# Kernel optimization log

Measured on AMD Instinct MI355X. Metric: run time of the kernel, lower is better.

The kernel has to match this reference:

```python
import jax, jax.numpy as jnp
import numpy as np

NUM_HEADS = 12
HEAD_DIM = 64
HIDDEN = 768
QMAX = 127.0  # 8-bit symmetric
DOMAIN_MIN, DOMAIN_MAX = -10.0, 0.0
NUM_INTERVALS = 12


def _build_pla_coeffs():
    xs = np.linspace(DOMAIN_MIN, DOMAIN_MAX, 1001)
    ys = np.exp(xs)
    intervals = np.linspace(DOMAIN_MIN, DOMAIN_MAX, NUM_INTERVALS + 1)
    ms, cs = [], []
    for i in range(NUM_INTERVALS):
        a, b = intervals[i], intervals[i + 1]
        mask = (xs >= a) & (xs <= b)
        m, c = np.polyfit(xs[mask], ys[mask], 1)
        ms.append(m)
        cs.append(c)
    return (jnp.asarray(ms, jnp.float32), jnp.asarray(cs, jnp.float32),
            jnp.asarray(intervals, jnp.float32))

COEFFS_M, COEFFS_C, INTERVALS = _build_pla_coeffs()


def quantize(x):
    # per-row (last-dim) abs-max symmetric 8-bit fake quant
    max_val = jnp.max(jnp.abs(x), axis=-1, keepdims=True)
    scale = max_val / QMAX
    scale = jnp.where(scale == 0, 1.0, scale)
    return jnp.clip(jnp.round(x / scale), -QMAX, QMAX) * scale


def to_fixed_point(x, bits=32, frac_bits=26):
    scale = 2.0 ** frac_bits
    lo = -2.0 ** (bits - 1)
    hi = 2.0 ** (bits - 1) - 1
    return jnp.clip(jnp.round(x * scale), lo, hi) / scale


def pla_exp(x):
    xc = jnp.clip(x, DOMAIN_MIN, DOMAIN_MAX)
    # sum(x >= intervals) - 1 == searchsorted(intervals, x, 'right') - 1
    idx = jnp.clip(jnp.searchsorted(INTERVALS, xc, side='right') - 1, 0, NUM_INTERVALS - 1)
    return COEFFS_M[idx] * xc + COEFFS_C[idx]


def pla_softmax(scores):
    shifted = scores - jnp.max(scores, axis=-1, keepdims=True)
    shifted_fx = to_fixed_point(shifted, 32, 26)
    exps = pla_exp(shifted_fx)
    sm = exps / (jnp.sum(exps, axis=-1, keepdims=True) + 1e-9)
    return quantize(sm)


def q_linear(x, W, b):
    # QuantizedLinear: quantize input and weight (per-row), fp bias
    return quantize(x) @ quantize(W).T + b


def split_heads(x):
    B, S, _ = x.shape
    return x.reshape(B, S, NUM_HEADS, HEAD_DIM).transpose(0, 2, 1, 3)  # bhsd


def mhsa(hidden_states, Wq, bq, Wk, bk, Wv, bv, Wo, bo):
    B, S, H = hidden_states.shape
    scale = HEAD_DIM ** -0.5
    q = split_heads(q_linear(hidden_states, Wq, bq))
    k = split_heads(q_linear(hidden_states, Wk, bk))
    v = split_heads(q_linear(hidden_states, Wv, bv))
    # per-row quantization makes tile-wise quant identical to full quant
    scores = jnp.einsum('bhqd,bhkd->bhqk', quantize(q), quantize(k)) * scale
    probs = pla_softmax(scores)
    ctx = jnp.einsum('bhqk,bhkd->bhqd', probs, quantize(v))
    ctx = ctx.transpose(0, 2, 1, 3).reshape(B, S, H)
    return q_linear(ctx, Wo, bo)


def setup_inputs() -> dict:
    key = jax.random.key(0)
    ks = jax.random.split(key, 9)
    B, S = 8, 512
    hs = jax.random.normal(ks[0], (B, S, HIDDEN), dtype=jnp.float32)
    def w(k):
        return jax.random.normal(k, (HIDDEN, HIDDEN), dtype=jnp.float32) * 0.02
    def b(k):
        return jax.random.normal(k, (HIDDEN,), dtype=jnp.float32) * 0.02
    return {
        'hidden_states': hs,
        'Wq': w(ks[1]), 'bq': b(ks[2]),
        'Wk': w(ks[3]), 'bk': b(ks[4]),
        'Wv': w(ks[5]), 'bv': b(ks[6]),
        'Wo': w(ks[7]), 'bo': b(ks[8]),
    }


def reference(hidden_states, Wq, bq, Wk, bk, Wv, bv, Wo, bo):
    return mhsa(hidden_states, Wq, bq, Wk, bk, Wv, bv, Wo, bo)
```

## Files before the change

### kernel.cpp

```cpp
#include <hip/hip_runtime.h>
#include <cmath>

#define R_TOT 4096
#define HID   768
#define NHEAD 12
#define HDIM  64
#define SEQ   512
#define BATCH 8

typedef int   v4i  __attribute__((ext_vector_type(4)));
typedef float v4f  __attribute__((ext_vector_type(4)));
typedef _Float16 half8 __attribute__((ext_vector_type(8)));
typedef _Float16 half4v __attribute__((ext_vector_type(4)));

__device__ __forceinline__ void gl_lds16(const signed char* g, signed char* l) {
  __builtin_amdgcn_global_load_lds(
      (const __attribute__((address_space(1))) void*)g,
      (__attribute__((address_space(3))) void*)l, 16, 0, 0);
}

struct PlaConsts { float m[12]; float c[12]; float b[13]; };

static PlaConsts build_pla() {
  PlaConsts pc;
  const int NPTS = 1001;
  static double xs[NPTS], ys[NPTS];
  const double step = 10.0 / 1000.0;
  for (int j = 0; j < NPTS; ++j) xs[j] = (double)j * step + (-10.0);
  xs[NPTS - 1] = 0.0;
  for (int j = 0; j < NPTS; ++j) ys[j] = std::exp(xs[j]);
  double bnd[13];
  const double step2 = 10.0 / 12.0;
  for (int k = 0; k < 13; ++k) bnd[k] = (double)k * step2 + (-10.0);
  bnd[12] = 0.0;
  for (int i = 0; i < 12; ++i) {
    const double a = bnd[i], bb = bnd[i + 1];
    double sx = 0, sy = 0; int n = 0;
    for (int j = 0; j < NPTS; ++j)
      if (xs[j] >= a && xs[j] <= bb) { sx += xs[j]; sy += ys[j]; ++n; }
    const double xm = sx / n, ym = sy / n;
    double sxx = 0, sxy = 0;
    for (int j = 0; j < NPTS; ++j)
      if (xs[j] >= a && xs[j] <= bb) {
        const double dx = xs[j] - xm;
        sxx += dx * dx; sxy += dx * (ys[j] - ym);
      }
    const double m = sxy / sxx;
    pc.m[i] = (float)m;
    pc.c[i] = (float)(ym - m * xm);
  }
  for (int k = 0; k < 13; ++k) pc.b[k] = (float)bnd[k];
  return pc;
}
static const PlaConsts g_pla = build_pla();

__device__ __forceinline__ void quant_row_wave(const float* __restrict__ x,
                                               signed char* __restrict__ qrow,
                                               float* __restrict__ srow) {
  const int lane = threadIdx.x & 63;
  const float4* x4 = (const float4*)x;
  const float4 a = x4[lane];
  const float4 b = x4[lane + 64];
  const float4 c = x4[lane + 128];
  float m = fmaxf(fmaxf(fabsf(a.x), fabsf(a.y)), fmaxf(fabsf(a.z), fabsf(a.w)));
  m = fmaxf(m, fmaxf(fmaxf(fabsf(b.x), fabsf(b.y)), fmaxf(fabsf(b.z), fabsf(b.w))));
  m = fmaxf(m, fmaxf(fmaxf(fabsf(c.x), fabsf(c.y)), fmaxf(fabsf(c.z), fabsf(c.w))));
  #pragma unroll
  for (int off = 32; off; off >>= 1) m = fmaxf(m, __shfl_xor(m, off));
  float s = m / 127.0f;
  if (s == 0.f) s = 1.f;
  auto qb = [&](float v) -> int {
    return ((int)fminf(fmaxf(rintf(v / s), -127.f), 127.f)) & 255;
  };
  const int p0 = qb(a.x) | (qb(a.y) << 8) | (qb(a.z) << 16) | (qb(a.w) << 24);
  const int p1 = qb(b.x) | (qb(b.y) << 8) | (qb(b.z) << 16) | (qb(b.w) << 24);
  const int p2 = qb(c.x) | (qb(c.y) << 8) | (qb(c.z) << 16) | (qb(c.w) << 24);
  int* q4 = (int*)qrow;
  q4[lane] = p0;
  q4[lane + 64] = p1;
  q4[lane + 128] = p2;
  if (lane == 0) *srow = s;
}

__global__ __launch_bounds__(256)
void quant_rows(const float* __restrict__ src,
                signed char* __restrict__ qout, float* __restrict__ sout) {
  const int row = blockIdx.x * 4 + (threadIdx.x >> 6);
  quant_row_wave(src + (size_t)row * HID, qout + (size_t)row * HID, sout + row);
}

__global__ __launch_bounds__(256)
void quant_all(const float* hs, const float* w0, const float* w1,
               const float* w2, const float* w3,
               signed char* qx, float* sx,
               signed char* q0, signed char* q1, signed char* q2, signed char* q3,
               float* s0, float* s1, float* s2, float* s3) {
  const int row = blockIdx.x * 4 + (threadIdx.x >> 6);
  const float* src; signed char* qo; float* so; int r;
  if (row < R_TOT)             { src = hs; qo = qx; so = sx; r = row; }
  else if (row < R_TOT + 768)  { src = w0; qo = q0; so = s0; r = row - R_TOT; }
  else if (row < R_TOT + 1536) { src = w1; qo = q1; so = s1; r = row - R_TOT - 768; }
  else if (row < R_TOT + 2304) { src = w2; qo = q2; so = s2; r = row - R_TOT - 1536; }
  else                         { src = w3; qo = q3; so = s3; r = row - R_TOT - 2304; }
  quant_row_wave(src + (size_t)r * HID, qo + (size_t)r * HID, so + r);
}

template <int NT>
__device__ __forceinline__
void proj_body(int mode,
               const signed char* __restrict__ qx, const float* __restrict__ sx,
               const signed char* __restrict__ qw, const float* __restrict__ sw,
               const float* __restrict__ bias,
               signed char* __restrict__ qo, float* __restrict__ so,
               _Float16* __restrict__ vt, float* __restrict__ fo,
               signed char* Al, signed char* Bl) {
  const int tid = threadIdx.x;
  const int w = tid >> 6, lane = tid & 63;
  const int n = lane & 15, quad = lane >> 4;
  const int row0 = blockIdx.x * 128, col0 = blockIdx.y * (NT * 16);
  const int lr = lane >> 3;
  const int lc = lane & 7;
  const int cg = lc ^ lr;
  v4i acc[2][NT];
  #pragma unroll
  for (int s = 0; s < 2; ++s)
    #pragma unroll
    for (int j = 0; j < NT; ++j) acc[s][j] = (v4i){0, 0, 0, 0};
  for (int k0 = 0; k0 < HID; k0 += 128) {
    if (k0) __syncthreads();
    #pragma unroll
    for (int m = 0; m < 4; ++m) {
      const int ci = w * 4 + m;
      gl_lds16(qx + (size_t)(row0 + ci * 8 + lr) * HID + k0 + cg * 16,
               Al + ci * 1024);
    }
    #pragma unroll
    for (int m = 0; m < NT / 2; ++m) {
      const int ci = w * (NT / 2) + m;
      gl_lds16(qw + (size_t)(col0 + ci * 8 + lr) * HID + k0 + cg * 16,
               Bl + ci * 1024);
    }
    __syncthreads();
    #pragma unroll
    for (int ks4 = 0; ks4 < 8; ks4 += 4) {
      const int sw16 = ((quad + ks4) ^ (n & 7)) * 16;
      const v4i af0 = *(const v4i*)&Al[(w * 16 + n) * 128 + sw16];
      const v4i af1 = *(const v4i*)&Al[(64 + w * 16 + n) * 128 + sw16];
      #pragma unroll
      for (int j = 0; j < NT; ++j) {
        const v4i bf = *(const v4i*)&Bl[(j * 16 + n) * 128 + sw16];
        acc[0][j] = __builtin_amdgcn_mfma_i32_16x16x64_i8(af0, bf, acc[0][j], 0, 0, 0);
        acc[1][j] = __builtin_amdgcn_mfma_i32_16x16x64_i8(af1, bf, acc[1][j], 0, 0, 0);
      }
    }
  }
  float swcv[NT], bcv[NT];
  #pragma unroll
  for (int j = 0; j < NT; ++j) {
    swcv[j] = sw[col0 + j * 16 + n];
    bcv[j] = bias[col0 + j * 16 + n];
  }
  #pragma unroll
  for (int s = 0; s < 2; ++s) {
    const int mrow = s * 64 + w * 16 + quad * 4;
    float sxr[4];
    #pragma unroll
    for (int r = 0; r < 4; ++r) sxr[r] = sx[row0 + mrow + r];
    float vals[NT][4];
    #pragma unroll
    for (int j = 0; j < NT; ++j)
      #pragma unroll
      for (int r = 0; r < 4; ++r)
        vals[j][r] = (float)acc[s][j][r] * (sxr[r] * swcv[j]) + bcv[j];
    if (mode == 1) {
      #pragma unroll
      for (int g = 0; g < NT / 4; ++g) {
        const int h = col0 / HDIM + g;
        #pragma unroll
        for (int r = 0; r < 4; ++r) {
          float m = 0.f;
          #pragma unroll
          for (int j = 0; j < 4; ++j) m = fmaxf(m, fabsf(vals[g * 4 + j][r]));
          #pragma unroll
          for (int off = 1; off < 16; off <<= 1) m = fmaxf(m, __shfl_xor(m, off));
          float sq = m / 127.0f;
          if (sq == 0.f) sq = 1.f;
          const int grow = row0 + mrow + r;
          const int bidx = grow >> 9, sidx = grow & 511;
          const size_t rowidx = ((size_t)bidx * NHEAD + h) * SEQ + sidx;
          #pragma unroll
          for (int j = 0; j < 4; ++j) {
            float q = fminf(fmaxf(rintf(vals[g * 4 + j][r] / sq), -127.f), 127.f);
            qo[rowidx * HDIM + j * 16 + n] = (signed char)(int)q;
          }
          if (n == 0) so[rowidx] = sq;
        }
      }
    } else if (mode == 2) {
      #pragma unroll
      for (int g = 0; g < NT / 4; ++g) {
        const int h = col0 / HDIM + g;
        float srow[4];
        #pragma unroll
        for (int r = 0; r < 4; ++r) {
          float m = 0.f;
          #pragma unroll
          for (int j = 0; j < 4; ++j) m = fmaxf(m, fabsf(vals[g * 4 + j][r]));
          #pragma unroll
          for (int off = 1; off < 16; off <<= 1) m = fmaxf(m, __shfl_xor(m, off));
          float sq = m / 127.0f;
          if (sq == 0.f) sq = 1.f;
          srow[r] = sq;
        }
        const int grow0 = row0 + mrow;
        const int bidx = grow0 >> 9, sidx = grow0 & 511;
        const int kb = sidx >> 5, ko = sidx & 31;
        const size_t hbv = (size_t)bidx * NHEAD + h;
        #pragma unroll
        for (int j = 0; j < 4; ++j) {
          half4v hv;
          #pragma unroll
          for (int r = 0; r < 4; ++r) {
            float q = fminf(fmaxf(rintf(vals[g * 4 + j][r] / srow[r]), -127.f), 127.f);
            hv[r] = (_Float16)(q * srow[r]);
          }
          *(half4v*)(vt + ((hbv * 16 + kb) * 64 + j * 16 + n) * 32 + ko) = hv;
        }
      }
    } else {
      #pragma unroll
      for (int r = 0; r < 4; ++r) {
        const size_t base = (size_t)(row0 + mrow + r) * HID + col0;
        #pragma unroll
        for (int j = 0; j < NT; ++j)
          fo[base + j * 16 + n] = vals[j][r];
      }
    }
  }
}

__global__ __launch_bounds__(256)
void proj_qkv(const signed char* __restrict__ qx, const float* __restrict__ sx,
              const signed char* qwq, const float* swq, const float* bq,
              signed char* qqd, float* qqs,
              const signed char* qwk, const float* swk, const float* bk,
              signed char* qkd, float* qks,
              const signed char* qwv, const float* swv, const float* bv,
              _Float16* vt2) {
  __shared__ __align__(16) signed char Al[128 * 128];
  __shared__ __align__(16) signed char Bl[128 * 128];
  if (blockIdx.z == 0)
    proj_body<8>(1, qx, sx, qwq, swq, bq, qqd, qqs, nullptr, nullptr, Al, Bl);
  else if (blockIdx.z == 1)
    proj_body<8>(1, qx, sx, qwk, swk, bk, qkd, qks, nullptr, nullptr, Al, Bl);
  else
    proj_body<8>(2, qx, sx, qwv, swv, bv, nullptr, nullptr, vt2, nullptr, Al, Bl);
}

__global__ __launch_bounds__(256)
void proj_out(const signed char* __restrict__ qx, const float* __restrict__ sx,
              const signed char* qw, const float* sw, const float* bias,
              float* fo) {
  __shared__ __align__(16) signed char Al[128 * 128];
  __shared__ __align__(16) signed char Bl[64 * 128];
  proj_body<4>(0, qx, sx, qw, sw, bias, nullptr, nullptr, nullptr, fo, Al, Bl);
}

__device__ __forceinline__
void softmax_exp_tile(float (&s)[8][4], float mx26, const float4* __restrict__ pt4,
                      float& sum_out, float& amax_out) {
  float sum = 0.f, amax = 0.f;
  #pragma unroll
  for (int t = 0; t < 8; ++t) {
    #pragma unroll
    for (int r = 0; r < 4; ++r) {
      float sh = s[t][r] - mx26;
      sh = fmaxf(sh, -671088640.0f);
      const float tq = rintf(sh);
      const float xc = tq * 1.4901161193847656e-08f;
      int g = (int)((xc + 10.0f) * 1.2f);
      g = g > 11 ? 11 : g;
      float4 E = pt4[g];
      int gn = g + ((xc >= E.y) ? 1 : 0) - ((xc < E.x) ? 1 : 0);
      gn = gn < 0 ? 0 : (gn > 11 ? 11 : gn);
      if (gn != g) E = pt4[gn];
      const float e = __fadd_rn(__fmul_rn(E.z, xc), E.w);
      s[t][r] = e;
      sum += e;
      amax = fmaxf(amax, fabsf(e));
    }
  }
  sum += __shfl_xor(sum, 16);
  sum += __shfl_xor(sum, 32);
  amax = fmaxf(amax, __shfl_xor(amax, 16));
  amax = fmaxf(amax, __shfl_xor(amax, 32));
  sum_out = sum; amax_out = amax;
}

__device__ __forceinline__
void quant_pack_tile(const float (&s)[8][4], float t127,
                     _Float16* __restrict__ phtrow, int w, int quad) {
  #pragma unroll
  for (int t = 0; t < 8; ++t) {
    half4v hq;
    #pragma unroll
    for (int r = 0; r < 4; ++r) {
      const float qf = fminf(fmaxf(rintf(s[t][r] * t127), -127.f), 127.f);
      hq[r] = (_Float16)qf;
    }
    *(half4v*)&phtrow[(t * 4 + w) * 16 + quad * 4] = hq;
  }
}

__device__ __forceinline__
v4f pv_tile(const _Float16* __restrict__ vbase, const _Float16* __restrict__ prow) {
  v4f acc = {0.f, 0.f, 0.f, 0.f};
  #pragma unroll
  for (int kt = 0; kt < 16; ++kt) {
    const half8 bf = *(const half8*)(vbase + kt * 2048);
    acc = __builtin_amdgcn_mfma_f32_16x16x32_f16(*(const half8*)(prow + kt * 32), bf, acc, 0, 0, 0);
  }
  return acc;
}

#define PSTR 520
__global__ __launch_bounds__(256)
void attn_kernel(const signed char* __restrict__ qq, const float* __restrict__ qss,
                 const signed char* __restrict__ qk, const float* __restrict__ kss,
                 const _Float16* __restrict__ vt2,
                 float* __restrict__ ctx, const PlaConsts pc) {
  __shared__ __align__(16) _Float16 PhT[2][16 * PSTR];
  __shared__ __align__(16) float red_max[2][16][4];
  __shared__ __align__(16) float red_sum[2][16][4];
  __shared__ __align__(16) float red_amax[2][16][4];
  __shared__ float psa[2][16];
  __shared__ __align__(16) float4 pt4[12];

  const int tid = threadIdx.x;
  const int q0 = blockIdx.x * 32;
  const int hh = blockIdx.y, bz = blockIdx.z;
  const size_t hb = (size_t)bz * NHEAD + hh;
  const signed char* qqh = qq + (hb * SEQ + q0) * HDIM;
  const signed char* qkh = qk + hb * SEQ * HDIM;
  const float* ksp = kss + hb * SEQ;

  if (tid < 12)
    pt4[tid] = make_float4(pc.b[tid], pc.b[tid + 1], pc.m[tid], pc.c[tid]);

  const int w = tid >> 6, lane = tid & 63;
  const int n = lane & 15, quad = lane >> 4;

  float s26[2][8][4];
  {
    const v4i qf0 = *(const v4i*)(qqh + (size_t)n * HDIM + quad * 16);
    const v4i qf1 = *(const v4i*)(qqh + (size_t)(16 + n) * HDIM + quad * 16);
    const float qs0 = (qss[hb * SEQ + q0 + n] * 0.125f) * 67108864.0f;
    const float qs1 = (qss[hb * SEQ + q0 + 16 + n] * 0.125f) * 67108864.0f;
    float vmax0 = -3.0e38f, vmax1 = -3.0e38f;
    #pragma unroll
    for (int t = 0; t < 8; ++t) {
      const int kc0 = (t * 4 + w) * 16;
      const v4i kfrag = *(const v4i*)(qkh + (size_t)(kc0 + n) * HDIM + quad * 16);
      const float4 ks4 = *(const float4*)(ksp + kc0 + quad * 4);
      v4i zero = {};
      const v4i a0 = __builtin_amdgcn_mfma_i32_16x16x64_i8(kfrag, qf0, zero, 0, 0, 0);
      const v4i a1 = __builtin_amdgcn_mfma_i32_16x16x64_i8(kfrag, qf1, zero, 0, 0, 0);
      const float ks[4] = {ks4.x, ks4.y, ks4.z, ks4.w};
      #pragma unroll
      for (int r = 0; r < 4; ++r) {
        const float v0 = (float)a0[r] * (qs0 * ks[r]);
        const float v1 = (float)a1[r] * (qs1 * ks[r]);
        s26[0][t][r] = v0; vmax0 = fmaxf(vmax0, v0);
        s26[1][t][r] = v1; vmax1 = fmaxf(vmax1, v1);
      }
    }
    vmax0 = fmaxf(vmax0, __shfl_xor(vmax0, 16));
    vmax0 = fmaxf(vmax0, __shfl_xor(vmax0, 32));
    vmax1 = fmaxf(vmax1, __shfl_xor(vmax1, 16));
    vmax1 = fmaxf(vmax1, __shfl_xor(vmax1, 32));
    if (quad == 0) { red_max[0][n][w] = vmax0; red_max[1][n][w] = vmax1; }
  }
  __syncthreads();

  {
    const float4 rm = *(const float4*)&red_max[0][n][0];
    const float mx26 = fmaxf(fmaxf(rm.x, rm.y), fmaxf(rm.z, rm.w));
    float sum, amax;
    softmax_exp_tile(s26[0], mx26, pt4, sum, amax);
    if (quad == 0) { red_sum[0][n][w] = sum; red_amax[0][n][w] = amax; }
  }
  __syncthreads();

  {
    const float4 rs = *(const float4*)&red_sum[0][n][0];
    const float4 ra = *(const float4*)&red_amax[0][n][0];
    float denom = (rs.x + rs.y) + (rs.z + rs.w);
    denom = __fadd_rn(denom, 1e-9f);
    const float rden = 1.0f / denom;
    const float am = fmaxf(fmaxf(ra.x, ra.y), fmaxf(ra.z, ra.w));
    float ps = (am * rden) / 127.0f;
    if (ps == 0.f) ps = 1.f;
    if (w == 0 && quad == 0) psa[0][n] = ps;
    const float t127 = 127.0f / am;
    quant_pack_tile(s26[0], t127, &PhT[0][n * PSTR], w, quad);

    const float4 rm = *(const float4*)&red_max[1][n][0];
    const float mx26 = fmaxf(fmaxf(rm.x, rm.y), fmaxf(rm.z, rm.w));
    float sum, amax;
    softmax_exp_tile(s26[1], mx26, pt4, sum, amax);
    if (quad == 0) { red_sum[1][n][w] = sum; red_amax[1][n][w] = amax; }
  }
  __syncthreads();

  const _Float16* vbase = vt2 + ((size_t)hb * 16 * 64 + (w * 16 + n)) * 32 + quad * 8;

  {
    const v4f acc0 = pv_tile(vbase, &PhT[0][n * PSTR + quad * 8]);

    const float4 rs = *(const float4*)&red_sum[1][n][0];
    const float4 ra = *(const float4*)&red_amax[1][n][0];
    float denom = (rs.x + rs.y) + (rs.z + rs.w);
    denom = __fadd_rn(denom, 1e-9f);
    const float rden = 1.0f / denom;
    const float am = fmaxf(fmaxf(ra.x, ra.y), fmaxf(ra.z, ra.w));
    float ps = (am * rden) / 127.0f;
    if (ps == 0.f) ps = 1.f;
    if (w == 0 && quad == 0) psa[1][n] = ps;
    const float t127 = 127.0f / am;
    quant_pack_tile(s26[1], t127, &PhT[1][n * PSTR], w, quad);

    #pragma unroll
    for (int r = 0; r < 4; ++r) {
      const int row = quad * 4 + r;
      ctx[((size_t)bz * SEQ + q0 + row) * HID + (size_t)hh * HDIM + w * 16 + n] =
          acc0[r] * psa[0][row];
    }
  }
  __syncthreads();

  {
    const v4f acc1 = pv_tile(vbase, &PhT[1][n * PSTR + quad * 8]);
    #pragma unroll
    for (int r = 0; r < 4; ++r) {
      const int row = quad * 4 + r;
      ctx[((size_t)bz * SEQ + q0 + 16 + row) * HID + (size_t)hh * HDIM + w * 16 + n] =
          acc1[r] * psa[1][row];
    }
  }
}

extern "C" void kernel_launch(void* const* d_in, const int* in_sizes, int n_in,
                              void* d_out, int out_size, void* d_ws, size_t ws_size,
                              hipStream_t stream) {
  (void)in_sizes; (void)n_in; (void)out_size; (void)ws_size;
  const float* hs = (const float*)d_in[0];
  const float* Wq = (const float*)d_in[1];
  const float* bq = (const float*)d_in[2];
  const float* Wk = (const float*)d_in[3];
  const float* bk = (const float*)d_in[4];
  const float* Wv = (const float*)d_in[5];
  const float* bv = (const float*)d_in[6];
  const float* Wo = (const float*)d_in[7];
  const float* bo = (const float*)d_in[8];
  float* out = (float*)d_out;

  char* ws = (char*)d_ws;
  size_t off = 0;
  auto alloc = [&](size_t bytes) -> char* {
    char* p = ws + off;
    off += (bytes + 255) & ~(size_t)255;
    return p;
  };
  signed char* qx  = (signed char*)alloc((size_t)R_TOT * HID);
  float*       sx  = (float*)alloc((size_t)R_TOT * 4);
  signed char* qwq = (signed char*)alloc((size_t)HID * HID);
  signed char* qwk = (signed char*)alloc((size_t)HID * HID);
  signed char* qwv = (signed char*)alloc((size_t)HID * HID);
  signed char* qwo = (signed char*)alloc((size_t)HID * HID);
  float*       swq = (float*)alloc((size_t)HID * 4);
  float*       swk = (float*)alloc((size_t)HID * 4);
  float*       swv = (float*)alloc((size_t)HID * 4);
  float*       swo = (float*)alloc((size_t)HID * 4);
  signed char* qqd = (signed char*)alloc((size_t)R_TOT * HID);
  float*       qqs = (float*)alloc((size_t)BATCH * NHEAD * SEQ * 4);
  signed char* qkd = (signed char*)alloc((size_t)R_TOT * HID);
  float*       qks = (float*)alloc((size_t)BATCH * NHEAD * SEQ * 4);
  float*       ctx = (float*)alloc((size_t)R_TOT * HID * 4);
  _Float16*    vt2 = (_Float16*)alloc((size_t)BATCH * NHEAD * HDIM * SEQ * 2);
  signed char* qc  = qx;
  float*       scs = sx;

  quant_all<<<(R_TOT + 4 * HID) / 4, 256, 0, stream>>>(
      hs, Wq, Wk, Wv, Wo, qx, sx,
      qwq, qwk, qwv, qwo, swq, swk, swv, swo);

  proj_qkv<<<dim3(R_TOT / 128, HID / 128, 3), 256, 0, stream>>>(
      qx, sx, qwq, swq, bq, qqd, qqs,
      qwk, swk, bk, qkd, qks,
      qwv, swv, bv, vt2);

  attn_kernel<<<dim3(SEQ / 32, NHEAD, BATCH), 256, 0, stream>>>(
      qqd, qqs, qkd, qks, vt2, ctx, g_pla);

  quant_rows<<<R_TOT / 4, 256, 0, stream>>>(ctx, qc, scs);
  proj_out<<<dim3(R_TOT / 128, HID / 64), 256, 0, stream>>>(
      qc, scs, qwo, swo, bo, out);
}
```

Measured before the change: 156.0 us.

## Double-buffer LDS in int8 projection GEMMs and shrink QKV column tile

Both projection kernels now double-buffer their LDS tiles. The next 128-wide K slice is loaded with global_load_lds while MFMAs run on the current slice, which removes one barrier per iteration. The QKV projection also drops from 128-column to 64-column tiles, one head per block, doubling its grid to raise occupancy and parallelism. The cost is more LDS per block (48KB), and each A tile is reloaded by twice as many blocks.

```diff
diff --git a/kernel.cpp b/kernel.cpp
--- a/kernel.cpp
+++ b/kernel.cpp
@@ -105,7 +105,26 @@
   quant_row_wave(src + (size_t)r * HID, qo + (size_t)r * HID, so + r);
 }
 
-template <int NT>
+__device__ __forceinline__
+void proj_stage(const signed char* __restrict__ qx,
+                const signed char* __restrict__ qw,
+                int row0, int col0, int k0,
+                signed char* __restrict__ Ab, signed char* __restrict__ Bb,
+                int w, int lr, int cg) {
+  #pragma unroll
+  for (int m = 0; m < 4; ++m) {
+    const int ci = w * 4 + m;
+    gl_lds16(qx + (size_t)(row0 + ci * 8 + lr) * HID + k0 + cg * 16,
+             Ab + ci * 1024);
+  }
+  #pragma unroll
+  for (int m = 0; m < 2; ++m) {
+    const int ci = w * 2 + m;
+    gl_lds16(qw + (size_t)(col0 + ci * 8 + lr) * HID + k0 + cg * 16,
+             Bb + ci * 1024);
+  }
+}
+
 __device__ __forceinline__
 void proj_body(int mode,
                const signed char* __restrict__ qx, const float* __restrict__ sx,
@@ -117,48 +136,47 @@
   const int tid = threadIdx.x;
   const int w = tid >> 6, lane = tid & 63;
   const int n = lane & 15, quad = lane >> 4;
-  const int row0 = blockIdx.x * 128, col0 = blockIdx.y * (NT * 16);
+  const int row0 = blockIdx.x * 128, col0 = blockIdx.y * 64;
   const int lr = lane >> 3;
   const int lc = lane & 7;
   const int cg = lc ^ lr;
-  v4i acc[2][NT];
+  v4i acc[2][4];
   #pragma unroll
   for (int s = 0; s < 2; ++s)
     #pragma unroll
-    for (int j = 0; j < NT; ++j) acc[s][j] = (v4i){0, 0, 0, 0};
-  for (int k0 = 0; k0 < HID; k0 += 128) {
-    if (k0) __syncthreads();
-    #pragma unroll
-    for (int m = 0; m < 4; ++m) {
-      const int ci = w * 4 + m;
-      gl_lds16(qx + (size_t)(row0 + ci * 8 + lr) * HID + k0 + cg * 16,
-               Al + ci * 1024);
-    }
-    #pragma unroll
-    for (int m = 0; m < NT / 2; ++m) {
-      const int ci = w * (NT / 2) + m;
-      gl_lds16(qw + (size_t)(col0 + ci * 8 + lr) * HID + k0 + cg * 16,
-               Bl + ci * 1024);
-    }
-    __syncthreads();
+    for (int j = 0; j < 4; ++j) acc[s][j] = (v4i){0, 0, 0, 0};
+
+  proj_stage(qx, qw, row0, col0, 0, Al, Bl, w, lr, cg);
+  __syncthreads();
+
+  #pragma unroll
+  for (int it = 0; it < 6; ++it) {
+    signed char* Ac = Al + (it & 1) * 16384;
+    signed char* Bc = Bl + (it & 1) * 8192;
+    if (it < 5)
+      proj_stage(qx, qw, row0, col0, (it + 1) * 128,
+                 Al + ((it & 1) ^ 1) * 16384, Bl + ((it & 1) ^ 1) * 8192,
+                 w, lr, cg);
     #pragma unroll
     for (int ks4 = 0; ks4 < 8; ks4 += 4) {
       const int sw16 = ((quad + ks4) ^ (n & 7)) * 16;
-      const v4i af0 = *(const v4i*)&Al[(w * 16 + n) * 128 + sw16];
-      const v4i af1 = *(const v4i*)&Al[(64 + w * 16 + n) * 128 + sw16];
-      #pragma unroll
-      for (int j = 0; j < NT; ++j) {
-        const v4i bf = *(const v4i*)&Bl[(j * 16 + n) * 128 + sw16];
+      const v4i af0 = *(const v4i*)&Ac[(w * 16 + n) * 128 + sw16];
+      const v4i af1 = *(const v4i*)&Ac[(64 + w * 16 + n) * 128 + sw16];
+      #pragma unroll
+      for (int j = 0; j < 4; ++j) {
+        const v4i bf = *(const v4i*)&Bc[(j * 16 + n) * 128 + sw16];
         acc[0][j] = __builtin_amdgcn_mfma_i32_16x16x64_i8(af0, bf, acc[0][j], 0, 0, 0);
         acc[1][j] = __builtin_amdgcn_mfma_i32_16x16x64_i8(af1, bf, acc[1][j], 0, 0, 0);
       }
     }
-  }
-  float swcv[NT], bcv[NT];
-  #pragma unroll
-  for (int j = 0; j < NT; ++j) {
-    swcv[j] = sw[col0 + j * 16 + n];
-    bcv[j] = bias[col0 + j * 16 + n];
+    if (it < 5) __syncthreads();
+  }
+
+  float swc4[4], bc4[4];
+  #pragma unroll
+  for (int j = 0; j < 4; ++j) {
+    swc4[j] = sw[col0 + j * 16 + n];
+    bc4[j] = bias[col0 + j * 16 + n];
   }
   #pragma unroll
   for (int s = 0; s < 2; ++s) {
@@ -166,73 +184,67 @@
     float sxr[4];
     #pragma unroll
     for (int r = 0; r < 4; ++r) sxr[r] = sx[row0 + mrow + r];
-    float vals[NT][4];
-    #pragma unroll
-    for (int j = 0; j < NT; ++j)
+    float vals[4][4];
+    #pragma unroll
+    for (int j = 0; j < 4; ++j)
       #pragma unroll
       for (int r = 0; r < 4; ++r)
-        vals[j][r] = (float)acc[s][j][r] * (sxr[r] * swcv[j]) + bcv[j];
+        vals[j][r] = (float)acc[s][j][r] * (sxr[r] * swc4[j]) + bc4[j];
     if (mode == 1) {
-      #pragma unroll
-      for (int g = 0; g < NT / 4; ++g) {
-        const int h = col0 / HDIM + g;
+      const int h = blockIdx.y;
+      #pragma unroll
+      for (int r = 0; r < 4; ++r) {
+        float m = 0.f;
+        #pragma unroll
+        for (int j = 0; j < 4; ++j) m = fmaxf(m, fabsf(vals[j][r]));
+        #pragma unroll
+        for (int off = 1; off < 16; off <<= 1) m = fmaxf(m, __shfl_xor(m, off));
+        float sq = m / 127.0f;
+        if (sq == 0.f) sq = 1.f;
+        const int grow = row0 + mrow + r;
+        const int bidx = grow >> 9, sidx = grow & 511;
+        const size_t rowidx = ((size_t)bidx * NHEAD + h) * SEQ + sidx;
+        #pragma unroll
+        for (int j = 0; j < 4; ++j) {
+          float q = fminf(fmaxf(rintf(vals[j][r] / sq), -127.f), 127.f);
+          qo[rowidx * HDIM + j * 16 + n] = (signed char)(int)q;
+        }
+        if (n == 0) so[rowidx] = sq;
+      }
+    } else if (mode == 2) {
+      const int h = blockIdx.y;
+      float srow[4];
+      #pragma unroll
+      for (int r = 0; r < 4; ++r) {
+        float m = 0.f;
+        #pragma unroll
+        for (int j = 0; j < 4; ++j) m = fmaxf(m, fabsf(vals[j][r]));
+        #pragma unroll
+        for (int off = 1; off < 16; off <<= 1) m = fmaxf(m, __shfl_xor(m, off));
+        float sq = m / 127.0f;
+        if (sq == 0.f) sq = 1.f;
+        srow[r] = sq;
+      }
+      const int grow0 = row0 + mrow;
+      const int bidx = grow0 >> 9, sidx = grow0 & 511;
+      const int kb = sidx >> 5, ko = sidx & 31;
+      const size_t hbv = (size_t)bidx * NHEAD + h;
+      #pragma unroll
+      for (int j = 0; j < 4; ++j) {
+        half4v hv;
         #pragma unroll
         for (int r = 0; r < 4; ++r) {
-          float m = 0.f;
-          #pragma unroll
-          for (int j = 0; j < 4; ++j) m = fmaxf(m, fabsf(vals[g * 4 + j][r]));
-          #pragma unroll
-          for (int off = 1; off < 16; off <<= 1) m = fmaxf(m, __shfl_xor(m, off));
-          float sq = m / 127.0f;
-          if (sq == 0.f) sq = 1.f;
-          const int grow = row0 + mrow + r;
-          const int bidx = grow >> 9, sidx = grow & 511;
-          const size_t rowidx = ((size_t)bidx * NHEAD + h) * SEQ + sidx;
-          #pragma unroll
-          for (int j = 0; j < 4; ++j) {
-            float q = fminf(fmaxf(rintf(vals[g * 4 + j][r] / sq), -127.f), 127.f);
-            qo[rowidx * HDIM + j * 16 + n] = (signed char)(int)q;
-          }
-          if (n == 0) so[rowidx] = sq;
+          float q = fminf(fmaxf(rintf(vals[j][r] / srow[r]), -127.f), 127.f);
+          hv[r] = (_Float16)(q * srow[r]);
         }
-      }
-    } else if (mode == 2) {
-      #pragma unroll
-      for (int g = 0; g < NT / 4; ++g) {
-        const int h = col0 / HDIM + g;
-        float srow[4];
-        #pragma unroll
-        for (int r = 0; r < 4; ++r) {
-          float m = 0.f;
-          #pragma unroll
-          for (int j = 0; j < 4; ++j) m = fmaxf(m, fabsf(vals[g * 4 + j][r]));
-          #pragma unroll
-          for (int off = 1; off < 16; off <<= 1) m = fmaxf(m, __shfl_xor(m, off));
-          float sq = m / 127.0f;
-          if (sq == 0.f) sq = 1.f;
-          srow[r] = sq;
-        }
-        const int grow0 = row0 + mrow;
-        const int bidx = grow0 >> 9, sidx = grow0 & 511;
-        const int kb = sidx >> 5, ko = sidx & 31;
-        const size_t hbv = (size_t)bidx * NHEAD + h;
-        #pragma unroll
-        for (int j = 0; j < 4; ++j) {
-          half4v hv;
-          #pragma unroll
-          for (int r = 0; r < 4; ++r) {
-            float q = fminf(fmaxf(rintf(vals[g * 4 + j][r] / srow[r]), -127.f), 127.f);
-            hv[r] = (_Float16)(q * srow[r]);
-          }
-          *(half4v*)(vt + ((hbv * 16 + kb) * 64 + j * 16 + n) * 32 + ko) = hv;
-        }
+        *(half4v*)(vt + ((hbv * 16 + kb) * 64 + j * 16 + n) * 32 + ko) = hv;
       }
     } else {
       #pragma unroll
       for (int r = 0; r < 4; ++r) {
         const size_t base = (size_t)(row0 + mrow + r) * HID + col0;
         #pragma unroll
-        for (int j = 0; j < NT; ++j)
+        for (int j = 0; j < 4; ++j)
           fo[base + j * 16 + n] = vals[j][r];
       }
     }
@@ -247,23 +259,23 @@
               signed char* qkd, float* qks,
               const signed char* qwv, const float* swv, const float* bv,
               _Float16* vt2) {
-  __shared__ __align__(16) signed char Al[128 * 128];
-  __shared__ __align__(16) signed char Bl[128 * 128];
+  __shared__ __align__(16) signed char Al[2 * 128 * 128];
+  __shared__ __align__(16) signed char Bl[2 * 64 * 128];
   if (blockIdx.z == 0)
-    proj_body<8>(1, qx, sx, qwq, swq, bq, qqd, qqs, nullptr, nullptr, Al, Bl);
+    proj_body(1, qx, sx, qwq, swq, bq, qqd, qqs, nullptr, nullptr, Al, Bl);
   else if (blockIdx.z == 1)
-    proj_body<8>(1, qx, sx, qwk, swk, bk, qkd, qks, nullptr, nullptr, Al, Bl);
+    proj_body(1, qx, sx, qwk, swk, bk, qkd, qks, nullptr, nullptr, Al, Bl);
   else
-    proj_body<8>(2, qx, sx, qwv, swv, bv, nullptr, nullptr, vt2, nullptr, Al, Bl);
+    proj_body(2, qx, sx, qwv, swv, bv, nullptr, nullptr, vt2, nullptr, Al, Bl);
 }
 
 __global__ __launch_bounds__(256)
 void proj_out(const signed char* __restrict__ qx, const float* __restrict__ sx,
               const signed char* qw, const float* sw, const float* bias,
               float* fo) {
-  __shared__ __align__(16) signed char Al[128 * 128];
-  __shared__ __align__(16) signed char Bl[64 * 128];
-  proj_body<4>(0, qx, sx, qw, sw, bias, nullptr, nullptr, nullptr, fo, Al, Bl);
+  __shared__ __align__(16) signed char Al[2 * 128 * 128];
+  __shared__ __align__(16) signed char Bl[2 * 64 * 128];
+  proj_body(0, qx, sx, qw, sw, bias, nullptr, nullptr, nullptr, fo, Al, Bl);
 }
 
 __device__ __forceinline__
@@ -494,7 +506,7 @@
       hs, Wq, Wk, Wv, Wo, qx, sx,
       qwq, qwk, qwv, qwo, swq, swk, swv, swo);
 
-  proj_qkv<<<dim3(R_TOT / 128, HID / 128, 3), 256, 0, stream>>>(
+  proj_qkv<<<dim3(R_TOT / 128, HID / 64, 3), 256, 0, stream>>>(
       qx, sx, qwq, swq, bq, qqd, qqs,
       qwk, swk, bk, qkd, qks,
       qwv, swv, bv, vt2);
```

Result: faster. 152.0 us (-2.6%).
